# Performance work log

Measured on AMD Instinct MI355X. Metric: run time of the kernel, lower is better.

## Reference

```python
import jax, jax.numpy as jnp
import numpy as np

B, T, C, H = 2, 2048, 1024, 16
D = C // H  # d_head = 64


def setup_inputs() -> dict:
    key = jax.random.key(0)
    k1, k2, k3 = jax.random.split(key, 3)
    x = jax.random.normal(k1, (B, T, C), dtype=jnp.float32)
    # torch Linear weights stored pre-transposed as [in, out] so we apply x @ W
    w_qkv = jax.random.normal(k2, (C, 3 * C), dtype=jnp.float32) * (C ** -0.5)
    w_out = jax.random.normal(k3, (C, C), dtype=jnp.float32) * (C ** -0.5)
    charge_w = jnp.array([0.0, 3.0, 6.0], dtype=jnp.float32)  # CHARGES init
    # causal mask, broadcast over batch and heads; mask==0 positions are blocked
    mask = jnp.tril(jnp.ones((1, 1, T, T), dtype=jnp.int32))
    return {"x": x, "mask": mask, "w_qkv": w_qkv, "w_out": w_out, "charge_w": charge_w}


def reference(x, mask, w_qkv, w_out, charge_w):
    B, T, C = x.shape
    H = 16
    D = C // H
    qkv = (x @ w_qkv).reshape(B, T, 3, H, D)
    q, k, v = qkv[:, :, 0], qkv[:, :, 1], qkv[:, :, 2]  # each [B,T,H,D]
    scale = D ** -0.5
    attn = jnp.einsum("bqhd,bkhd->bhqk", q, k) * scale  # [B,H,T,T]
    charge_bias = jnp.mod(jnp.sum(charge_w), 9.0) * 0.001  # scalar bias
    attn = attn + charge_bias
    attn = jnp.where(mask == 0, jnp.float32(-1e9), attn)
    attn = jax.nn.softmax(attn, axis=-1)  # dropout is identity in eval mode
    out = jnp.einsum("bhqk,bkhd->bqhd", attn, v).reshape(B, T, C)
    return out @ w_out
```

## Files before the change

kernel.cpp:

```cpp
#include <hip/hip_runtime.h>
#include <stdint.h>


typedef __attribute__((ext_vector_type(4))) float f32x4;
typedef __attribute__((ext_vector_type(16))) float f32x16;
typedef __attribute__((ext_vector_type(8))) __bf16 bf16x8;
typedef __attribute__((ext_vector_type(8))) unsigned short ushort8;
typedef __attribute__((ext_vector_type(4))) unsigned short ushort4v;
typedef __attribute__((ext_vector_type(4))) unsigned int uint4v;

#define DEV __device__ __forceinline__

DEV unsigned short f32_to_bf16(float f) {
    union { float f; unsigned int u; } cv; cv.f = f;
    unsigned int u = cv.u;
    return (unsigned short)((u + 0x7FFFu + ((u >> 16) & 1u)) >> 16);
}

DEV float bf16_to_f32(unsigned short u) {
    union { unsigned int i; float f; } cv; cv.i = ((unsigned int)u) << 16;
    return cv.f;
}

DEV bf16x8 load_bf16x8(const unsigned short* p) {
    ushort8 v = *(const ushort8*)p;
    return __builtin_bit_cast(bf16x8, v);
}

DEV unsigned cvt_pk_bf16(float lo, float hi) {
    unsigned r;
    asm("v_cvt_pk_bf16_f32 %0, %1, %2" : "=v"(r) : "v"(lo), "v"(hi));
    return r;
}

DEV void gload_lds16(const void* g, void* l) {
    __builtin_amdgcn_global_load_lds(
        (const __attribute__((address_space(1))) unsigned int*)g,
        (__attribute__((address_space(3))) unsigned int*)l, 16, 0, 0);
}

DEV f32x16 vzero16() {
    f32x16 v;
#pragma unroll
    for (int i = 0; i < 16; ++i) v[i] = 0.f;
    return v;
}

DEV float tmax32(const f32x16& a, const f32x16& b) {
    float m[16];
#pragma unroll
    for (int i = 0; i < 16; ++i) m[i] = fmaxf(a[i], b[i]);
#pragma unroll
    for (int st = 8; st > 0; st >>= 1)
#pragma unroll
        for (int i = 0; i < 8; ++i) if (i < st) m[i] = fmaxf(m[i], m[i + st]);
    return m[0];
}
DEV float tsum32(const f32x16& a, const f32x16& b) {
    float m[16];
#pragma unroll
    for (int i = 0; i < 16; ++i) m[i] = a[i] + b[i];
#pragma unroll
    for (int st = 8; st > 0; st >>= 1)
#pragma unroll
        for (int i = 0; i < 8; ++i) if (i < st) m[i] = m[i] + m[i + st];
    return m[0];
}

__device__ __constant__ unsigned char qQ[32]  = { 6, 5,14,14,14,13, 9, 9, 4,13,13,12,12, 8, 8,15,15,15,15,12,11,11,11,10, 7, 7, 3,10,10, 2, 1, 0};
__device__ __constant__ unsigned char tsQ[32] = { 0, 0, 0,10,20, 0, 0,10, 0,10,19, 0, 9, 0, 9, 0, 8,16,24,18, 0, 8,16, 0, 0, 8, 0, 8,15, 0, 0, 0};
__device__ __constant__ unsigned char teQ[32] = {14,12,10,20,30,10,10,20,10,19,28, 9,18, 9,18, 8,16,24,32,26, 8,16,24, 8, 8,16, 8,15,22, 6, 4, 2};
__device__ __constant__ unsigned char mlQ[32] = {255,255, 4, 5, 6, 7,19,20,255, 8, 9,10,11,21,22, 0, 1, 2, 3,12,13,14,15,16,23,24,255,17,18,255,255,255};
__device__ __constant__ unsigned char obQ[32] = {255,255,255, 3, 4,255,255,13,255, 5, 6,255, 7,255,14,255, 0, 1, 2, 8,255, 9,10,255,255,15,255,11,12,255,255,255};
__device__ __constant__ unsigned char ncs[9]  = {4,3,3,3,3,3,2,2,2};
__device__ __constant__ unsigned char mlbs[9] = {0,4,7,10,13,16,19,21,23};
__device__ __constant__ unsigned char obbs[9] = {0,3,5,7,9,11,13,14,15};

__global__ __launch_bounds__(256) void prep_kernel(const float* __restrict__ x,
                                                   const float* __restrict__ w_qkv,
                                                   const float* __restrict__ w_out,
                                                   unsigned short* __restrict__ xb,
                                                   unsigned short* __restrict__ wqkvT,
                                                   unsigned short* __restrict__ woutT) {
    __shared__ float tl[32][33];
    const int bx = blockIdx.x;
    const int tid = threadIdx.x;
    if (bx < 2048) {
        int i = (bx * 256 + tid) * 8;
        f32x4 a = *(const f32x4*)(x + i);
        f32x4 b = *(const f32x4*)(x + i + 4);
        ushort8 o;
        o[0] = f32_to_bf16(a[0]); o[1] = f32_to_bf16(a[1]);
        o[2] = f32_to_bf16(a[2]); o[3] = f32_to_bf16(a[3]);
        o[4] = f32_to_bf16(b[0]); o[5] = f32_to_bf16(b[1]);
        o[6] = f32_to_bf16(b[2]); o[7] = f32_to_bf16(b[3]);
        *(ushort8*)(xb + i) = o;
        return;
    }
    const float* in;
    unsigned short* out;
    int R, Cn, c0, r0;
    if (bx < 5120) {
        int idx = bx - 2048;
        in = w_qkv; out = wqkvT; R = 1024; Cn = 3072;
        c0 = (idx % 96) * 32; r0 = (idx / 96) * 32;
    } else {
        int idx = bx - 5120;
        in = w_out; out = woutT; R = 1024; Cn = 1024;
        c0 = (idx % 32) * 32; r0 = (idx / 32) * 32;
    }
    const int tx = tid & 31, ty = tid >> 5;
#pragma unroll
    for (int rr = 0; rr < 4; ++rr) {
        int r = ty + rr * 8;
        tl[r][tx] = in[(size_t)(r0 + r) * Cn + c0 + tx];
    }
    __syncthreads();
#pragma unroll
    for (int rr = 0; rr < 4; ++rr) {
        int cc = ty + rr * 8;
        out[(size_t)(c0 + cc) * R + r0 + tx] = f32_to_bf16(tl[tx][cc]);
    }
}

template<bool OUT_BF16, bool SCALE_Q>
__global__ __launch_bounds__(256) void gemm_kernel(
    const unsigned short* __restrict__ A,
    const unsigned short* __restrict__ Bt,
    void* __restrict__ C, int K, int ldc)
{
    __shared__ __align__(16) unsigned short As[3][4096];
    __shared__ __align__(16) unsigned short Bs[3][4096];

    const int tid = threadIdx.x;
    const int lane = tid & 63;
    const int w = tid >> 6;
    const int wr = w >> 1, wc = w & 1;
    const int g = lane >> 4, ci = lane & 15;
    const int nwg = gridDim.x * gridDim.y;
    const int lid = blockIdx.y * gridDim.x + blockIdx.x;
    const int swz = (lid & 7) * (nwg >> 3) + (lid >> 3);
    const int bx = swz % gridDim.x, by = swz / gridDim.x;
    const int soff = w * 1024 + lane * 16;
    const int srow = soff >> 6;
    const int scch = (soff >> 4) & 3;

#define GSTAGE(buf, k0_) do { \
    _Pragma("unroll") for (int i_ = 0; i_ < 2; ++i_) { \
        int row_ = srow + i_ * 64; \
        gload_lds16(A  + (size_t)(by * 128 + row_) * K + (k0_) + scch * 8, \
                    (char*)As[buf] + i_ * 4096 + w * 1024); \
        gload_lds16(Bt + (size_t)(bx * 128 + row_) * K + (k0_) + scch * 8, \
                    (char*)Bs[buf] + i_ * 4096 + w * 1024); } } while (0)

    f32x4 acc[4][4];
#pragma unroll
    for (int i = 0; i < 4; ++i)
#pragma unroll
        for (int j = 0; j < 4; ++j) acc[i][j] = f32x4{0.f, 0.f, 0.f, 0.f};

    const int nk = K >> 5;
    GSTAGE(0, 0);
    GSTAGE(1, 32);
    asm volatile("s_waitcnt vmcnt(4)" ::: "memory");
    __builtin_amdgcn_sched_barrier(0);
    __builtin_amdgcn_s_barrier();
    __builtin_amdgcn_sched_barrier(0);

    for (int kt = 0; kt < nk; ++kt) {
        const int cur = kt % 3;
        if (kt + 2 < nk) GSTAGE((kt + 2) % 3, (kt + 2) << 5);

        bf16x8 af[4], bfr[4];
#pragma unroll
        for (int mf = 0; mf < 4; ++mf) af[mf]  = load_bf16x8(&As[cur][(wr * 64 + mf * 16 + ci) * 32 + g * 8]);
#pragma unroll
        for (int nf = 0; nf < 4; ++nf) bfr[nf] = load_bf16x8(&Bs[cur][(wc * 64 + nf * 16 + ci) * 32 + g * 8]);
        __builtin_amdgcn_s_setprio(1);
#pragma unroll
        for (int mf = 0; mf < 4; ++mf)
#pragma unroll
            for (int nf = 0; nf < 4; ++nf)
                acc[mf][nf] = __builtin_amdgcn_mfma_f32_16x16x32_bf16(af[mf], bfr[nf], acc[mf][nf], 0, 0, 0);
        __builtin_amdgcn_s_setprio(0);

        if (kt + 2 < nk) asm volatile("s_waitcnt vmcnt(4) lgkmcnt(0)" ::: "memory");
        else             asm volatile("s_waitcnt vmcnt(0) lgkmcnt(0)" ::: "memory");
        __builtin_amdgcn_sched_barrier(0);
        __builtin_amdgcn_s_barrier();
        __builtin_amdgcn_sched_barrier(0);
    }
#undef GSTAGE

#pragma unroll
    for (int mf = 0; mf < 4; ++mf)
#pragma unroll
        for (int nf = 0; nf < 4; ++nf)
#pragma unroll
            for (int r = 0; r < 4; ++r) {
                int row = by * 128 + wr * 64 + mf * 16 + g * 4 + r;
                int col = bx * 128 + wc * 64 + nf * 16 + ci;
                float v = acc[mf][nf][r];
                if (SCALE_Q && col < 1024) v *= 0.1803368801f;
                if (OUT_BF16)
                    ((unsigned short*)C)[(size_t)row * ldc + col] = f32_to_bf16(v);
                else
                    ((float*)C)[(size_t)row * ldc + col] = v;
            }
}

__global__ __launch_bounds__(256) void attn7_kernel(const unsigned short* __restrict__ qkv,
                                                    unsigned short* __restrict__ attn,
                                                    unsigned short* __restrict__ Obuf,
                                                    float* __restrict__ mlbuf) {
    constexpr int T = 2048, HD3 = 3072, Cc = 1024;
    __shared__ __align__(16) unsigned short Ks[3][4096];
    __shared__ __align__(16) unsigned short Vt[2][4096];

    const int tid = threadIdx.x;
    const int lane = tid & 63;
    const int w = tid >> 6;
    const int l31 = lane & 31;
    const int hi = lane >> 5;

    const int bx = blockIdx.x;
    const int j = bx >> 5;
    const int bh = bx & 31;
    const int q = qQ[j];
    const int ts = tsQ[j], te = teQ[j];
    const int h = bh & 15;
    const int b = bh >> 4;
    const int q0w = q * 128 + w * 32;
    const int qrow = q0w + l31;
    const size_t base = (size_t)b * T * HD3;
    const int ntc = te - ts;

    bf16x8 qf[4];
#pragma unroll
    for (int t = 0; t < 4; ++t)
        qf[t] = load_bf16x8(qkv + base + (size_t)qrow * HD3 + h * 64 + t * 16 + hi * 8);

    f32x16 acc0 = vzero16(), acc1 = vzero16();
    float m = -3e38f, l = 0.f;

    ushort8 vA0, vA1, vB0, vB1;
#define LOADV(tile, r0, r1) do { int kv0_ = (tile) * 64; \
    int rr0_ = tid >> 3, cc0_ = tid & 7; \
    r0 = *(const ushort8*)(qkv + base + (size_t)(kv0_ + rr0_) * HD3 + 2 * Cc + h * 64 + cc0_ * 8); \
    int c1_ = 256 + tid; int rr1_ = c1_ >> 3, cc1_ = c1_ & 7; \
    r1 = *(const ushort8*)(qkv + base + (size_t)(kv0_ + rr1_) * HD3 + 2 * Cc + h * 64 + cc1_ * 8); } while (0)

#define DMAK(tile, kb) do { int kv0_ = (tile) * 64; \
    _Pragma("unroll") for (int i_ = 0; i_ < 2; ++i_) { \
        int off_ = i_ * 4096 + w * 1024 + lane * 16; \
        int row_ = off_ >> 7; \
        int csw_ = ((lane & 7) * 8) ^ ((row_ & 7) * 8); \
        gload_lds16(qkv + base + (size_t)(kv0_ + row_) * HD3 + Cc + h * 64 + csw_, \
                    (void*)(((char*)&Ks[kb][0]) + i_ * 4096 + w * 1024)); } } while (0)

#define WRITEV(vb, r0, r1) do { \
    _Pragma("unroll") for (int i_ = 0; i_ < 2; ++i_) { \
        int c_ = i_ * 256 + tid; int row_ = c_ >> 3, cc_ = c_ & 7; \
        ushort8 v_ = i_ ? r1 : r0; \
        _Pragma("unroll") for (int j_ = 0; j_ < 8; ++j_) { \
            int d_ = cc_ * 8 + j_; \
            int sw_ = ((d_ ^ (d_ >> 3)) & 7) * 8; \
            Vt[vb][d_ * 64 + (row_ ^ sw_)] = v_[j_]; } } } while (0)

    LOADV(ts, vA0, vA1);
    DMAK(ts, 0);
    asm volatile("s_waitcnt vmcnt(0)" ::: "memory");
    __builtin_amdgcn_sched_barrier(0);
    WRITEV(0, vA0, vA1);
    LOADV(ts + 1, vB0, vB1);
    DMAK(ts + 1, 1);
    asm volatile("s_waitcnt lgkmcnt(0)" ::: "memory");
    __builtin_amdgcn_sched_barrier(0);
    __builtin_amdgcn_s_barrier();
    __builtin_amdgcn_sched_barrier(0);

    for (int tt = 0; tt < ntc; ++tt) {
        const int t = ts + tt;
        const int kv0 = t * 64;
        const int kcur = tt % 3;
        const int vcur = tt & 1;
        const bool act = (kv0 <= q0w + 31);
        const bool pre2 = (tt + 2) < ntc;

        if (tt + 1 < ntc) {
            if (tt & 1) WRITEV(vcur ^ 1, vA0, vA1); else WRITEV(vcur ^ 1, vB0, vB1);
        }
        if (pre2) {
            if (tt & 1) LOADV(t + 2, vB0, vB1); else LOADV(t + 2, vA0, vA1);
            DMAK(t + 2, (tt + 2) % 3);
        }

        if (act) {
            f32x16 s0 = vzero16(), s1 = vzero16();
            bf16x8 pf[4];
            const bool st1_ok = (kv0 + 32 <= q0w + 31);
            __builtin_amdgcn_s_setprio(1);
#pragma unroll
            for (int tf = 0; tf < 4; ++tf) {
                int row = l31;
                int idx = kcur * 4096 + row * 64 + ((tf * 16 + hi * 8) ^ ((row & 7) * 8));
                s0 = __builtin_amdgcn_mfma_f32_32x32x16_bf16(load_bf16x8(&Ks[0][idx]), qf[tf], s0, 0, 0, 0);
            }
            if (st1_ok) {
#pragma unroll
                for (int tf = 0; tf < 4; ++tf) {
                    int row = 32 + l31;
                    int idx = kcur * 4096 + row * 64 + ((tf * 16 + hi * 8) ^ ((row & 7) * 8));
                    s1 = __builtin_amdgcn_mfma_f32_32x32x16_bf16(load_bf16x8(&Ks[0][idx]), qf[tf], s1, 0, 0, 0);
                }
            }
            __builtin_amdgcn_s_setprio(0);
            const bool needmask = (kv0 + 63 > q0w);
            if (needmask) {
#pragma unroll
                for (int G = 0; G < 4; ++G)
#pragma unroll
                    for (int rr = 0; rr < 4; ++rr) {
                        int kvb = kv0 + 8 * G + 4 * hi + rr;
                        s0[G * 4 + rr] = (kvb      <= qrow) ? s0[G * 4 + rr] : -3e38f;
                        s1[G * 4 + rr] = (kvb + 32 <= qrow) ? s1[G * 4 + rr] : -3e38f;
                    }
            }
            float pmax = tmax32(s0, s1);
            pmax = fmaxf(pmax, __shfl_xor(pmax, 32));
            if (!__all(pmax - m <= 11.5f)) {
                float mnew = fmaxf(m, pmax);
                float alpha = exp2f(m - mnew);
                m = mnew;
                l *= alpha;
#pragma unroll
                for (int i = 0; i < 16; ++i) { acc0[i] *= alpha; acc1[i] *= alpha; }
            }
#pragma unroll
            for (int i = 0; i < 16; ++i) {
                s0[i] = exp2f(s0[i] - m);
                s1[i] = exp2f(s1[i] - m);
            }

            unsigned pk0[4][2], pk1[4][2];
#pragma unroll
            for (int G = 0; G < 4; ++G) {
                pk0[G][0] = cvt_pk_bf16(s0[G * 4 + 0], s0[G * 4 + 1]);
                pk0[G][1] = cvt_pk_bf16(s0[G * 4 + 2], s0[G * 4 + 3]);
                pk1[G][0] = cvt_pk_bf16(s1[G * 4 + 0], s1[G * 4 + 1]);
                pk1[G][1] = cvt_pk_bf16(s1[G * 4 + 2], s1[G * 4 + 3]);
            }
#pragma unroll
            for (int tf = 0; tf < 4; ++tf) {
                const int kb = tf & 1;
                unsigned sA0, sA1, sB0, sB1;
                if (tf < 2) { sA0 = pk0[2 * kb][0]; sA1 = pk0[2 * kb][1]; sB0 = pk0[2 * kb + 1][0]; sB1 = pk0[2 * kb + 1][1]; }
                else        { sA0 = pk1[2 * kb][0]; sA1 = pk1[2 * kb][1]; sB0 = pk1[2 * kb + 1][0]; sB1 = pk1[2 * kb + 1][1]; }
                unsigned sd0 = hi ? sA0 : sB0, sd1 = hi ? sA1 : sB1;
                unsigned rc0 = (unsigned)__shfl_xor((int)sd0, 32);
                unsigned rc1 = (unsigned)__shfl_xor((int)sd1, 32);
                uint4v u;
                u[0] = hi ? rc0 : sA0;  u[1] = hi ? rc1 : sA1;
                u[2] = hi ? sB0 : rc0;  u[3] = hi ? sB1 : rc1;
                pf[tf] = __builtin_bit_cast(bf16x8, u);
            }

            __builtin_amdgcn_s_setprio(1);
#pragma unroll
            for (int tf = 0; tf < 4; ++tf) {
                {
                    int d = l31, sw = ((d ^ (d >> 3)) & 7) * 8;
                    bf16x8 vf = load_bf16x8(&Vt[vcur][d * 64 + ((tf * 16 + hi * 8) ^ sw)]);
                    acc0 = __builtin_amdgcn_mfma_f32_32x32x16_bf16(vf, pf[tf], acc0, 0, 0, 0);
                }
                {
                    int d = 32 + l31, sw = ((d ^ (d >> 3)) & 7) * 8;
                    bf16x8 vf = load_bf16x8(&Vt[vcur][d * 64 + ((tf * 16 + hi * 8) ^ sw)]);
                    acc1 = __builtin_amdgcn_mfma_f32_32x32x16_bf16(vf, pf[tf], acc1, 0, 0, 0);
                }
            }
            __builtin_amdgcn_s_setprio(0);

            float rsum = tsum32(s0, s1);
            l += rsum + __shfl_xor(rsum, 32);
        }

        if (pre2) asm volatile("s_waitcnt vmcnt(4) lgkmcnt(0)" ::: "memory");
        else      asm volatile("s_waitcnt vmcnt(0) lgkmcnt(0)" ::: "memory");
        __builtin_amdgcn_sched_barrier(0);
        __builtin_amdgcn_s_barrier();
        __builtin_amdgcn_sched_barrier(0);
    }

    const int mlq = mlQ[j], obq = obQ[j];
    if (mlq == 255) {
        const float invl = 1.0f / l;
        const size_t ob = (size_t)b * T * Cc + (size_t)qrow * Cc + h * 64;
#pragma unroll
        for (int G = 0; G < 4; ++G) {
            ushort4v o0, o1;
#pragma unroll
            for (int rr = 0; rr < 4; ++rr) {
                o0[rr] = f32_to_bf16(acc0[G * 4 + rr] * invl);
                o1[rr] = f32_to_bf16(acc1[G * 4 + rr] * invl);
            }
            int d0 = 8 * G + 4 * hi;
            *(ushort4v*)(attn + ob + d0) = o0;
            *(ushort4v*)(attn + ob + 32 + d0) = o1;
        }
    } else {
        const int qlocal = w * 32 + l31;
        unsigned short* op = (obq == 255)
            ? (attn + (size_t)b * T * Cc + (size_t)qrow * Cc + h * 64)
            : (Obuf + (size_t)(bh * 16 + obq) * 8192 + qlocal * 64);
#pragma unroll
        for (int G = 0; G < 4; ++G) {
            ushort4v o0, o1;
#pragma unroll
            for (int rr = 0; rr < 4; ++rr) {
                o0[rr] = f32_to_bf16(acc0[G * 4 + rr]);
                o1[rr] = f32_to_bf16(acc1[G * 4 + rr]);
            }
            int d0 = 8 * G + 4 * hi;
            *(ushort4v*)(op + d0) = o0;
            *(ushort4v*)(op + 32 + d0) = o1;
        }
        if (hi == 0) {
            float* mp = mlbuf + (size_t)(bh * 25 + mlq) * 256 + qlocal * 2;
            mp[0] = m; mp[1] = l;
        }
    }
#undef LOADV
#undef DMAK
#undef WRITEV
}

__global__ __launch_bounds__(256) void combine3_kernel(const unsigned short* __restrict__ Obuf,
                                                       const float* __restrict__ mlbuf,
                                                       unsigned short* __restrict__ attn) {
    constexpr int T = 2048, Cc = 1024;
    const int ss = blockIdx.x;
    const int bh = ss / 9, s = ss - bh * 9;
    const int q = 15 - s;
    const int nc = ncs[s], mlb = mlbs[s], obb = obbs[s];
    const int b = bh >> 4, h = bh & 15;
    const int tid = threadIdx.x;
    const int qlocal = tid >> 1, dh = (tid & 1) * 32;

    float mv[4], lv[4];
#pragma unroll
    for (int c = 0; c < 4; ++c) {
        mv[c] = -3e38f; lv[c] = 0.f;
        if (c < nc) {
            const float* mp = mlbuf + (size_t)(bh * 25 + mlb + c) * 256 + qlocal * 2;
            mv[c] = mp[0]; lv[c] = mp[1];
        }
    }
    float M = fmaxf(fmaxf(mv[0], mv[1]), fmaxf(mv[2], mv[3]));
    float fc[4];
    float denom = 0.f;
#pragma unroll
    for (int c = 0; c < 4; ++c) {
        fc[c] = (c < nc) ? exp2f(mv[c] - M) : 0.f;
        denom += fc[c] * lv[c];
    }
    const float inv = 1.f / denom;
#pragma unroll
    for (int c = 0; c < 4; ++c) fc[c] *= inv;

    unsigned short* po = attn + (size_t)b * T * Cc + (size_t)(q * 128 + qlocal) * Cc + h * 64 + dh;
#pragma unroll
    for (int i = 0; i < 4; ++i) {
        float acc[8] = {0.f, 0.f, 0.f, 0.f, 0.f, 0.f, 0.f, 0.f};
#pragma unroll
        for (int c = 0; c < 4; ++c) {
            if (c < nc) {
                const unsigned short* pc = (c == 0)
                    ? po
                    : (Obuf + (size_t)(bh * 16 + obb + c - 1) * 8192 + qlocal * 64 + dh);
                ushort8 a = *(const ushort8*)(pc + i * 8);
#pragma unroll
                for (int k = 0; k < 8; ++k) acc[k] += fc[c] * bf16_to_f32(a[k]);
            }
        }
        ushort8 o;
#pragma unroll
        for (int k = 0; k < 8; ++k) o[k] = f32_to_bf16(acc[k]);
        *(ushort8*)(po + i * 8) = o;
    }
}

extern "C" void kernel_launch(void* const* d_in, const int* in_sizes, int n_in,
                              void* d_out, int out_size, void* d_ws, size_t ws_size,
                              hipStream_t stream) {
    const float* x     = (const float*)d_in[0];
    const float* w_qkv = (const float*)d_in[2];
    const float* w_out = (const float*)d_in[3];
    float* out = (float*)d_out;

    unsigned short* xb     = (unsigned short*)d_ws;
    unsigned short* wqkvT  = xb + 4194304;
    unsigned short* woutT  = wqkvT + 3145728;
    unsigned short* qkv    = woutT + 1048576;
    unsigned short* attn   = qkv + 12582912;
    unsigned short* Obuf   = xb;
    float*          mlbuf  = (float*)wqkvT;

    prep_kernel<<<6144, 256, 0, stream>>>(x, w_qkv, w_out, xb, wqkvT, woutT);

    gemm_kernel<true, true><<<dim3(24, 32), 256, 0, stream>>>(xb, wqkvT, (void*)qkv, 1024, 3072);

    attn7_kernel<<<1024, 256, 0, stream>>>(qkv, attn, Obuf, mlbuf);
    combine3_kernel<<<288, 256, 0, stream>>>(Obuf, mlbuf, attn);

    gemm_kernel<false, false><<<dim3(8, 32), 256, 0, stream>>>(attn, woutT, (void*)out, 1024, 1024);
}
```

Baseline: 133.5 us.

## Split attention into finer KV chunks and double-buffer K for higher occupancy

Reworks the causal attention work split from 32 to 40 chunk assignments per (batch, head), so the longer query blocks are divided into more, shorter KV ranges. The combine step now merges partials for 12 query blocks instead of 9. K shared memory drops from triple to double buffering, with K prefetched one tile ahead rather than two, and a launch bound of 5 blocks per CU is requested to raise occupancy. The aim is better load balance across CUs and more resident waves. The cost is more partial outputs to write and combine, and a shorter K prefetch distance that may expose more load latency.

```diff
diff --git a/kernel.cpp b/kernel.cpp
--- a/kernel.cpp
+++ b/kernel.cpp
@@ -67,14 +67,14 @@
     return m[0];
 }
 
-__device__ __constant__ unsigned char qQ[32]  = { 6, 5,14,14,14,13, 9, 9, 4,13,13,12,12, 8, 8,15,15,15,15,12,11,11,11,10, 7, 7, 3,10,10, 2, 1, 0};
-__device__ __constant__ unsigned char tsQ[32] = { 0, 0, 0,10,20, 0, 0,10, 0,10,19, 0, 9, 0, 9, 0, 8,16,24,18, 0, 8,16, 0, 0, 8, 0, 8,15, 0, 0, 0};
-__device__ __constant__ unsigned char teQ[32] = {14,12,10,20,30,10,10,20,10,19,28, 9,18, 9,18, 8,16,24,32,26, 8,16,24, 8, 8,16, 8,15,22, 6, 4, 2};
-__device__ __constant__ unsigned char mlQ[32] = {255,255, 4, 5, 6, 7,19,20,255, 8, 9,10,11,21,22, 0, 1, 2, 3,12,13,14,15,16,23,24,255,17,18,255,255,255};
-__device__ __constant__ unsigned char obQ[32] = {255,255,255, 3, 4,255,255,13,255, 5, 6,255, 7,255,14,255, 0, 1, 2, 8,255, 9,10,255,255,15,255,11,12,255,255,255};
-__device__ __constant__ unsigned char ncs[9]  = {4,3,3,3,3,3,2,2,2};
-__device__ __constant__ unsigned char mlbs[9] = {0,4,7,10,13,16,19,21,23};
-__device__ __constant__ unsigned char obbs[9] = {0,3,5,7,9,11,13,14,15};
+__device__ __constant__ unsigned char qN[40]  = {15,15,15,15,14,14,11,11,11,10, 7, 7, 3,14,14,13,13,13,13,12,12,10,10, 9, 9, 6, 6,12,12, 9, 8, 8, 8, 5, 5, 2, 4, 4, 1, 0};
+__device__ __constant__ unsigned char tsN[40] = { 0, 8,16,24, 0, 8, 0, 8,16, 0, 0, 8, 0,16,23, 0, 7,14,21, 0, 7, 8,15, 0, 7, 0, 7,14,20,14, 0, 6,12, 0, 6, 0, 0, 5, 0, 0};
+__device__ __constant__ unsigned char teN[40] = { 8,16,24,32, 8,16, 8,16,24, 8, 8,16, 8,23,30, 7,14,21,28, 7,14,15,22, 7,14, 7,14,20,26,20, 6,12,18, 6,12, 6, 5,10, 4, 2};
+__device__ __constant__ unsigned char mlN[40] = { 0, 1, 2, 3, 4, 5,16,17,18,19,28,29,255, 6, 7, 8, 9,10,11,12,13,20,21,22,23,30,31,14,15,24,25,26,27,32,33,255,34,35,255,255};
+__device__ __constant__ unsigned char obN[40] = {255, 0, 1, 2,255, 3,255,12,13,255,255,20,255, 4, 5,255, 6, 7, 8,255, 9,14,15,255,16,255,21,10,11,17,255,18,19,255,22,255,255,23,255,255};
+__device__ __constant__ unsigned char nc12[12]   = {4,4,4,4,3,3,3,3,2,2,2,2};
+__device__ __constant__ unsigned char mlbs12[12] = {0,4,8,12,16,19,22,25,28,30,32,34};
+__device__ __constant__ unsigned char obbs12[12] = {0,3,6,9,12,14,16,18,20,21,22,23};
 
 __global__ __launch_bounds__(256) void prep_kernel(const float* __restrict__ x,
                                                    const float* __restrict__ w_qkv,
@@ -209,12 +209,12 @@
             }
 }
 
-__global__ __launch_bounds__(256) void attn7_kernel(const unsigned short* __restrict__ qkv,
-                                                    unsigned short* __restrict__ attn,
-                                                    unsigned short* __restrict__ Obuf,
-                                                    float* __restrict__ mlbuf) {
+__global__ __launch_bounds__(256, 5) void attn9_kernel(const unsigned short* __restrict__ qkv,
+                                                       unsigned short* __restrict__ attn,
+                                                       unsigned short* __restrict__ Obuf,
+                                                       float* __restrict__ mlbuf) {
     constexpr int T = 2048, HD3 = 3072, Cc = 1024;
-    __shared__ __align__(16) unsigned short Ks[3][4096];
+    __shared__ __align__(16) unsigned short Ks[2][4096];
     __shared__ __align__(16) unsigned short Vt[2][4096];
 
     const int tid = threadIdx.x;
@@ -226,8 +226,8 @@
     const int bx = blockIdx.x;
     const int j = bx >> 5;
     const int bh = bx & 31;
-    const int q = qQ[j];
-    const int ts = tsQ[j], te = teQ[j];
+    const int q = qN[j];
+    const int ts = tsN[j], te = teN[j];
     const int h = bh & 15;
     const int b = bh >> 4;
     const int q0w = q * 128 + w * 32;
@@ -273,7 +273,6 @@
     __builtin_amdgcn_sched_barrier(0);
     WRITEV(0, vA0, vA1);
     LOADV(ts + 1, vB0, vB1);
-    DMAK(ts + 1, 1);
     asm volatile("s_waitcnt lgkmcnt(0)" ::: "memory");
     __builtin_amdgcn_sched_barrier(0);
     __builtin_amdgcn_s_barrier();
@@ -282,17 +281,18 @@
     for (int tt = 0; tt < ntc; ++tt) {
         const int t = ts + tt;
         const int kv0 = t * 64;
-        const int kcur = tt % 3;
+        const int kcur = tt & 1;
         const int vcur = tt & 1;
         const bool act = (kv0 <= q0w + 31);
-        const bool pre2 = (tt + 2) < ntc;
-
-        if (tt + 1 < ntc) {
+        const bool preK = (tt + 1) < ntc;
+        const bool preV = (tt + 2) < ntc;
+
+        if (preK) {
             if (tt & 1) WRITEV(vcur ^ 1, vA0, vA1); else WRITEV(vcur ^ 1, vB0, vB1);
         }
-        if (pre2) {
+        if (preK) DMAK(t + 1, kcur ^ 1);
+        if (preV) {
             if (tt & 1) LOADV(t + 2, vB0, vB1); else LOADV(t + 2, vA0, vA1);
-            DMAK(t + 2, (tt + 2) % 3);
         }
 
         if (act) {
@@ -385,14 +385,14 @@
             l += rsum + __shfl_xor(rsum, 32);
         }
 
-        if (pre2) asm volatile("s_waitcnt vmcnt(4) lgkmcnt(0)" ::: "memory");
+        if (preV) asm volatile("s_waitcnt vmcnt(2) lgkmcnt(0)" ::: "memory");
         else      asm volatile("s_waitcnt vmcnt(0) lgkmcnt(0)" ::: "memory");
         __builtin_amdgcn_sched_barrier(0);
         __builtin_amdgcn_s_barrier();
         __builtin_amdgcn_sched_barrier(0);
     }
 
-    const int mlq = mlQ[j], obq = obQ[j];
+    const int mlq = mlN[j], obq = obN[j];
     if (mlq == 255) {
         const float invl = 1.0f / l;
         const size_t ob = (size_t)b * T * Cc + (size_t)qrow * Cc + h * 64;
@@ -412,7 +412,7 @@
         const int qlocal = w * 32 + l31;
         unsigned short* op = (obq == 255)
             ? (attn + (size_t)b * T * Cc + (size_t)qrow * Cc + h * 64)
-            : (Obuf + (size_t)(bh * 16 + obq) * 8192 + qlocal * 64);
+            : (Obuf + (size_t)(bh * 24 + obq) * 8192 + qlocal * 64);
 #pragma unroll
         for (int G = 0; G < 4; ++G) {
             ushort4v o0, o1;
@@ -426,7 +426,7 @@
             *(ushort4v*)(op + 32 + d0) = o1;
         }
         if (hi == 0) {
-            float* mp = mlbuf + (size_t)(bh * 25 + mlq) * 256 + qlocal * 2;
+            float* mp = mlbuf + (size_t)(bh * 36 + mlq) * 256 + qlocal * 2;
             mp[0] = m; mp[1] = l;
         }
     }
@@ -435,14 +435,14 @@
 #undef WRITEV
 }
 
-__global__ __launch_bounds__(256) void combine3_kernel(const unsigned short* __restrict__ Obuf,
+__global__ __launch_bounds__(256) void combine5_kernel(const unsigned short* __restrict__ Obuf,
                                                        const float* __restrict__ mlbuf,
                                                        unsigned short* __restrict__ attn) {
     constexpr int T = 2048, Cc = 1024;
     const int ss = blockIdx.x;
-    const int bh = ss / 9, s = ss - bh * 9;
+    const int bh = ss / 12, s = ss - bh * 12;
     const int q = 15 - s;
-    const int nc = ncs[s], mlb = mlbs[s], obb = obbs[s];
+    const int nc = nc12[s], mlb = mlbs12[s], obb = obbs12[s];
     const int b = bh >> 4, h = bh & 15;
     const int tid = threadIdx.x;
     const int qlocal = tid >> 1, dh = (tid & 1) * 32;
@@ -452,7 +452,7 @@
     for (int c = 0; c < 4; ++c) {
         mv[c] = -3e38f; lv[c] = 0.f;
         if (c < nc) {
-            const float* mp = mlbuf + (size_t)(bh * 25 + mlb + c) * 256 + qlocal * 2;
+            const float* mp = mlbuf + (size_t)(bh * 36 + mlb + c) * 256 + qlocal * 2;
             mv[c] = mp[0]; lv[c] = mp[1];
         }
     }
@@ -477,7 +477,7 @@
             if (c < nc) {
                 const unsigned short* pc = (c == 0)
                     ? po
-                    : (Obuf + (size_t)(bh * 16 + obb + c - 1) * 8192 + qlocal * 64 + dh);
+                    : (Obuf + (size_t)(bh * 24 + obb + c - 1) * 8192 + qlocal * 64 + dh);
                 ushort8 a = *(const ushort8*)(pc + i * 8);
 #pragma unroll
                 for (int k = 0; k < 8; ++k) acc[k] += fc[c] * bf16_to_f32(a[k]);
@@ -504,14 +504,14 @@
     unsigned short* qkv    = woutT + 1048576;
     unsigned short* attn   = qkv + 12582912;
     unsigned short* Obuf   = xb;
-    float*          mlbuf  = (float*)wqkvT;
+    float*          mlbuf  = (float*)(xb + 6291456);
 
     prep_kernel<<<6144, 256, 0, stream>>>(x, w_qkv, w_out, xb, wqkvT, woutT);
 
     gemm_kernel<true, true><<<dim3(24, 32), 256, 0, stream>>>(xb, wqkvT, (void*)qkv, 1024, 3072);
 
-    attn7_kernel<<<1024, 256, 0, stream>>>(qkv, attn, Obuf, mlbuf);
-    combine3_kernel<<<288, 256, 0, stream>>>(Obuf, mlbuf, attn);
+    attn9_kernel<<<1280, 256, 0, stream>>>(qkv, attn, Obuf, mlbuf);
+    combine5_kernel<<<384, 256, 0, stream>>>(Obuf, mlbuf, attn);
 
     gemm_kernel<false, false><<<dim3(8, 32), 256, 0, stream>>>(attn, woutT, (void*)out, 1024, 1024);
 }
```

New measurement: 285.2 us. 114% more time.
